# Performance work log

Measured on AMD Instinct MI355X. Metric: run time of the kernel, lower is better.

## Reference

```python
import jax, jax.numpy as jnp
import numpy as np

B, T, D = 2, 1024, 1024
E, H, TOPK = 32, 256, 4
S, HS = 2, H * TOPK  # shared experts, shared hidden dim


def setup_inputs() -> dict:
    key = jax.random.key(0)
    ks = jax.random.split(key, 10)
    sc = 0.02
    return {
        "x": jax.random.normal(ks[0], (B, T, D), dtype=jnp.float32),
        "Wr": jax.random.normal(ks[1], (E, D), dtype=jnp.float32) * sc,
        "router_bias": jnp.zeros((E,), dtype=jnp.float32),
        "Wg": jax.random.normal(ks[2], (E, H, D), dtype=jnp.float32) * sc,
        "Wu": jax.random.normal(ks[3], (E, H, D), dtype=jnp.float32) * sc,
        "Wd": jax.random.normal(ks[4], (E, D, H), dtype=jnp.float32) * sc,
        "Sg": jax.random.normal(ks[5], (S, HS, D), dtype=jnp.float32) * sc,
        "Su": jax.random.normal(ks[6], (S, HS, D), dtype=jnp.float32) * sc,
        "Sd": jax.random.normal(ks[7], (S, D, HS), dtype=jnp.float32) * sc,
    }


def reference(x, Wr, router_bias, Wg, Wu, Wd, Sg, Su, Sd):
    Bx, Tx, Dx = x.shape
    flat = x.reshape(-1, Dx)                      # [N, D]
    N = flat.shape[0]

    # Router: softmax over raw logits, top-k selection on biased logits
    logits = flat @ Wr.T                          # [N, E]
    scores = jax.nn.softmax(logits, axis=-1)
    _, topk_idx = jax.lax.top_k(logits + router_bias, TOPK)   # [N, K]
    topk_scores = jnp.take_along_axis(scores, topk_idx, axis=-1)
    topk_scores = topk_scores / jnp.sum(topk_scores, axis=-1, keepdims=True)

    # Dense per-token per-expert combine weights (0 for unselected experts)
    cw = jnp.zeros((N, E), dtype=flat.dtype).at[
        jnp.arange(N)[:, None], topk_idx
    ].add(topk_scores)                            # [N, E]

    # Routed experts: SwiGLU applied per expert, zero-weighted if unselected
    g = jnp.einsum("nd,ehd->neh", flat, Wg)       # [N, E, H]
    u = jnp.einsum("nd,ehd->neh", flat, Wu)
    h = jax.nn.silu(g) * u
    hw = h * cw[:, :, None]                       # fold combine weight before down-proj
    out = jnp.einsum("neh,edh->nd", hw, Wd)       # [N, D]

    # Shared experts: always active, summed on top
    gs = jnp.einsum("nd,shd->nsh", flat, Sg)      # [N, S, HS]
    us = jnp.einsum("nd,shd->nsh", flat, Su)
    hs = jax.nn.silu(gs) * us
    out = out + jnp.einsum("nsh,sdh->nd", hs, Sd)

    return out.reshape(Bx, Tx, Dx)
```

## Files before the change

### kernel.cpp

```cpp
#include <hip/hip_runtime.h>
#include <hip/hip_bf16.h>


#define N_TOK 2048
#define DDIM 1024
#define NEXP 32
#define HDIM 256
#define TOPK 4
#define NSH 2
#define HSH 1024
#define CNTS 32
#define WM2  96

typedef unsigned short us4 __attribute__((ext_vector_type(4)));
typedef unsigned short us8 __attribute__((ext_vector_type(8)));
typedef short bf16x8 __attribute__((ext_vector_type(8)));
typedef float f32x4 __attribute__((ext_vector_type(4)));

__device__ __forceinline__ unsigned short f2bf(float f) {
  union { float f; unsigned u; } v; v.f = f;
  unsigned r = v.u + 0x7fffu + ((v.u >> 16) & 1u);
  return (unsigned short)(r >> 16);
}
__device__ __forceinline__ float bf2f(unsigned short h) {
  union { unsigned u; float f; } v; v.u = ((unsigned)h) << 16; return v.f;
}
__device__ __forceinline__ uint2 cvt4u(float4 v) {
  union { __hip_bfloat162 b; unsigned u; } a, b2;
  a.b  = __float22bfloat162_rn(make_float2(v.x, v.y));
  b2.b = __float22bfloat162_rn(make_float2(v.z, v.w));
  return make_uint2(a.u, b2.u);
}

__device__ __forceinline__ void pipe_barrier() {
  asm volatile("s_waitcnt lgkmcnt(0)" ::: "memory");
  __builtin_amdgcn_s_barrier();
  __builtin_amdgcn_sched_barrier(0);
}

#define C_X4   524288L
#define C_WG4  2621440L
#define C_WU4  4718592L
#define C_WD4  6815744L
#define C_SG4  7340032L
#define C_SU4  7864320L
#define C_TOT4 8388608L
#define NCVT   16384

__global__ __launch_bounds__(256) void k_prep(const float* __restrict__ x,
                                              const float* __restrict__ Wr,
                                              const float* __restrict__ rb,
                                              const float* __restrict__ Wg,
                                              const float* __restrict__ Wu,
                                              const float* __restrict__ Wd,
                                              const float* __restrict__ Sg,
                                              const float* __restrict__ Su,
                                              const float* __restrict__ Sd,
                                              unsigned short* __restrict__ xb,
                                              unsigned short* __restrict__ Wgb,
                                              unsigned short* __restrict__ Wub,
                                              unsigned short* __restrict__ Wdb,
                                              unsigned short* __restrict__ Sgb,
                                              unsigned short* __restrict__ Sub,
                                              unsigned short* __restrict__ Sdb,
                                              int* __restrict__ cnt,
                                              int* __restrict__ ent,
                                              float* __restrict__ wgt) {
  __shared__ float sX[8 * 1024];
  __shared__ float sLog[8 * 32];
  int tid = threadIdx.x;
  if (blockIdx.x >= 256) {
    long base = (long)(blockIdx.x - 256) * 512;
    const float* s; unsigned short* d; long off;
    if (base < C_WG4) {
      if (base < C_X4)  { s = x;  d = xb;  off = base; }
      else              { s = Wg; d = Wgb; off = base - C_X4; }
    } else if (base < C_WD4) {
      if (base < C_WU4) { s = Wu; d = Wub; off = base - C_WG4; }
      else              { s = Wd; d = Wdb; off = base - C_WU4; }
    } else if (base < C_SU4) {
      if (base < C_SG4) { s = Sg; d = Sgb; off = base - C_WD4; }
      else              { s = Su; d = Sub; off = base - C_SG4; }
    } else              { s = Sd; d = Sdb; off = base - C_SU4; }
    long i0 = off + 2 * tid;
    float4 v0 = reinterpret_cast<const float4*>(s)[i0];
    float4 v1 = reinterpret_cast<const float4*>(s)[i0 + 1];
    uint2 a = cvt4u(v0), b = cvt4u(v1);
    uint4 o = make_uint4(a.x, a.y, b.x, b.y);
    reinterpret_cast<uint4*>(d)[(off >> 1) + tid] = o;
    return;
  }
  int blk = blockIdx.x;
  {
    const float4* xsrc = reinterpret_cast<const float4*>(x + (size_t)blk * 8 * 1024);
    float4* xdst = reinterpret_cast<float4*>(sX);
#pragma unroll
    for (int i = 0; i < 8; i++) xdst[tid + 256 * i] = xsrc[tid + 256 * i];
  }
  __syncthreads();
  int tloc = tid >> 5, e = tid & 31;
  const float4* wr4 = reinterpret_cast<const float4*>(Wr + (size_t)e * DDIM);
  const float* xr = sX + tloc * 1024;
  float acc = 0.f;
#pragma unroll 8
  for (int d4 = 0; d4 < 256; d4++) {
    float4 wv = wr4[d4];
    acc += xr[d4 * 4 + 0] * wv.x + xr[d4 * 4 + 1] * wv.y +
           xr[d4 * 4 + 2] * wv.z + xr[d4 * 4 + 3] * wv.w;
  }
  sLog[tloc * 32 + e] = acc;
  __syncthreads();
  if (tid < 8) {
    int tok = blk * 8 + tid;
    const float* lg = sLog + tid * 32;
    int usedmask = 0;
    int idx[TOPK]; float lv[TOPK];
#pragma unroll
    for (int k = 0; k < TOPK; k++) {
      float best = -3.4e38f; int bi = 0;
      for (int ee = 0; ee < NEXP; ee++) {
        if ((usedmask >> ee) & 1) continue;
        float v = lg[ee] + rb[ee];
        if (v > best) { best = v; bi = ee; }
      }
      usedmask |= 1 << bi; idx[k] = bi; lv[k] = lg[bi];
    }
    float m = fmaxf(fmaxf(lv[0], lv[1]), fmaxf(lv[2], lv[3]));
    float w[TOPK]; float ssum = 0.f;
#pragma unroll
    for (int k = 0; k < TOPK; k++) { w[k] = __expf(lv[k] - m); ssum += w[k]; }
    float inv = 1.f / ssum;
#pragma unroll
    for (int k = 0; k < TOPK; k++) {
      int ee = idx[k];
      int pos = atomicAdd(&cnt[ee * CNTS], 1);
      ent[ee * N_TOK + pos] = tok * TOPK + k;
      wgt[ee * N_TOK + pos] = w[k] * inv;
    }
  }
}

__global__ void k_plan(const int* __restrict__ cnt, int* __restrict__ wk2, int* __restrict__ nwk2) {
  int e = threadIdx.x;
  if (e >= 32) return;
  int ne = cnt[e * CNTS];
  int nt2 = (ne + 127) >> 7;
  int off2 = 0;
  for (int j = 0; j < 32; j++) {
    int v2 = __shfl(nt2, j);
    if (j < e) off2 += v2;
  }
  for (int t = 0; t < nt2; t++) wk2[off2 + t] = e | (t << 8);
  if (e == 31) nwk2[0] = off2 + nt2;
}

__global__ __launch_bounds__(512) void k_gu(const unsigned short* __restrict__ xb,
                                            const unsigned short* __restrict__ Sgb,
                                            const unsigned short* __restrict__ Sub,
                                            const unsigned short* __restrict__ Wgb,
                                            const unsigned short* __restrict__ Wub,
                                            const int* __restrict__ cnt,
                                            const int* __restrict__ ent,
                                            const float* __restrict__ wgt,
                                            unsigned short* __restrict__ hs,
                                            unsigned short* __restrict__ hw,
                                            const int* __restrict__ wk2,
                                            const int* __restrict__ nwk2) {
  __shared__ unsigned short sPool[2 * 128 * 40 + 2 * 256 * 40];
  __shared__ int sTok[128];
  __shared__ float sW[128];
  int tid = threadIdx.x, lane = tid & 63, wid = tid >> 6;
  int wm = wid >> 2, wn = wid & 3;
  int b = blockIdx.x;

  if (b < 256) {
    int xg = b & 15, mt = b >> 4;
    int s = xg >> 3, ht = xg & 7;
    unsigned short* sA = sPool;
    unsigned short* sB = sPool + 2 * 128 * 40;

    int ar = tid >> 2, akc = tid & 3;
    const unsigned short* aSrc = xb + (size_t)(mt * 128 + ar) * DDIM + akc * 8;
    int aOff = ar * 40 + akc * 8;
    const unsigned short* bSrc[2];
    int bOff[2];
#pragma unroll
    for (int p = 0; p < 2; p++) {
      int c = tid + p * 512;
      int row = c >> 2, kc = c & 3;
      int sel = (row >> 4) & 1;
      int h = ht * 128 + ((row >> 5) << 4) + (row & 15);
      bSrc[p] = (sel ? Sub : Sgb) + (size_t)(s * HSH + h) * DDIM + kc * 8;
      bOff[p] = row * 40 + kc * 8;
    }

    us8 aReg = *reinterpret_cast<const us8*>(aSrc);
    us8 bReg[2];
#pragma unroll
    for (int p = 0; p < 2; p++) bReg[p] = *reinterpret_cast<const us8*>(bSrc[p]);

    f32x4 acc[4][4];
#pragma unroll
    for (int mf = 0; mf < 4; mf++)
#pragma unroll
      for (int nf = 0; nf < 4; nf++) acc[mf][nf] = {0.f, 0.f, 0.f, 0.f};

    int cur = 0;
    for (int step = 0; step < 32; ++step) {
      *reinterpret_cast<us8*>(&sA[cur * 5120 + aOff]) = aReg;
#pragma unroll
      for (int p = 0; p < 2; p++) *reinterpret_cast<us8*>(&sB[cur * 10240 + bOff[p]]) = bReg[p];
      if (step < 31) {
        int k0 = (step + 1) * 32;
        aReg = *reinterpret_cast<const us8*>(aSrc + k0);
#pragma unroll
        for (int p = 0; p < 2; p++) bReg[p] = *reinterpret_cast<const us8*>(bSrc[p] + k0);
      }
      pipe_barrier();
      int ka = (lane >> 4) * 8;
      bf16x8 a[4];
#pragma unroll
      for (int mf = 0; mf < 4; mf++)
        a[mf] = *reinterpret_cast<const bf16x8*>(&sA[cur * 5120 + (wm * 64 + mf * 16 + (lane & 15)) * 40 + ka]);
#pragma unroll
      for (int nf = 0; nf < 4; nf++) {
        bf16x8 bb = *reinterpret_cast<const bf16x8*>(&sB[cur * 10240 + (wn * 64 + nf * 16 + (lane & 15)) * 40 + ka]);
#pragma unroll
        for (int mf = 0; mf < 4; mf++)
          acc[mf][nf] = __builtin_amdgcn_mfma_f32_16x16x32_bf16(a[mf], bb, acc[mf][nf], 0, 0, 0);
      }
      cur ^= 1;
    }
#pragma unroll
    for (int mf = 0; mf < 4; mf++) {
#pragma unroll
      for (int t = 0; t < 2; t++) {
#pragma unroll
        for (int r = 0; r < 4; r++) {
          int tok = mt * 128 + wm * 64 + mf * 16 + ((lane >> 4) << 2) + r;
          float g = acc[mf][2 * t][r], u = acc[mf][2 * t + 1][r];
          float hval = (g / (1.f + __expf(-g))) * u;
          int h = ht * 128 + (wn * 2 + t) * 16 + (lane & 15);
          hs[(size_t)(tok * NSH + s) * HSH + h] = f2bf(hval);
        }
      }
    }
    return;
  }

  int idx = b - 256;
  int widx = idx >> 2, ht = idx & 3;
  if (widx >= nwk2[0]) return;
  int item = wk2[widx];
  int e = item & 255, mt = item >> 8;
  int ne = cnt[e * CNTS];
  unsigned short* sA = sPool;
  unsigned short* sB = sPool + 2 * 128 * 40;
  if (tid < 128) {
    int pos = mt * 128 + tid;
    int p2 = min(pos, ne - 1);
    sTok[tid] = ent[e * N_TOK + p2];
    sW[tid] = (pos < ne) ? wgt[e * N_TOK + p2] : 0.f;
  }
  __syncthreads();

  int ar = tid >> 2, akc = tid & 3;
  const unsigned short* aSrc = xb + (size_t)(sTok[ar] >> 2) * DDIM + akc * 8;
  int aOff = ar * 40 + akc * 8;
  int br = tid >> 2, bkc = tid & 3;
  int sel = (br >> 4) & 1;
  int h = ht * 64 + ((br >> 5) << 4) + (br & 15);
  const unsigned short* bSrc = (sel ? Wub : Wgb) + (size_t)(e * HDIM + h) * DDIM + bkc * 8;
  int bOff = br * 40 + bkc * 8;

  us8 aReg = *reinterpret_cast<const us8*>(aSrc);
  us8 bReg = *reinterpret_cast<const us8*>(bSrc);

  f32x4 acc[4][2];
#pragma unroll
  for (int mf = 0; mf < 4; mf++)
#pragma unroll
    for (int nf = 0; nf < 2; nf++) acc[mf][nf] = {0.f, 0.f, 0.f, 0.f};

  int cur = 0;
  for (int step = 0; step < 32; ++step) {
    *reinterpret_cast<us8*>(&sA[cur * 5120 + aOff]) = aReg;
    *reinterpret_cast<us8*>(&sB[cur * 5120 + bOff]) = bReg;
    if (step < 31) {
      int k0 = (step + 1) * 32;
      aReg = *reinterpret_cast<const us8*>(aSrc + k0);
      bReg = *reinterpret_cast<const us8*>(bSrc + k0);
    }
    pipe_barrier();
    int ka = (lane >> 4) * 8;
    bf16x8 a[4];
#pragma unroll
    for (int mf = 0; mf < 4; mf++)
      a[mf] = *reinterpret_cast<const bf16x8*>(&sA[cur * 5120 + (wm * 64 + mf * 16 + (lane & 15)) * 40 + ka]);
#pragma unroll
    for (int nf = 0; nf < 2; nf++) {
      bf16x8 bb = *reinterpret_cast<const bf16x8*>(&sB[cur * 5120 + (wn * 32 + nf * 16 + (lane & 15)) * 40 + ka]);
#pragma unroll
      for (int mf = 0; mf < 4; mf++)
        acc[mf][nf] = __builtin_amdgcn_mfma_f32_16x16x32_bf16(a[mf], bb, acc[mf][nf], 0, 0, 0);
    }
    cur ^= 1;
  }
#pragma unroll
  for (int mf = 0; mf < 4; mf++) {
#pragma unroll
    for (int r = 0; r < 4; r++) {
      int tl = wm * 64 + mf * 16 + ((lane >> 4) << 2) + r;
      int pos = mt * 128 + tl;
      if (pos < ne) {
        float g = acc[mf][0][r], u = acc[mf][1][r];
        float hval = (g / (1.f + __expf(-g))) * u * sW[tl];
        int ts = sTok[tl];
        int hcol = ht * 64 + wn * 16 + (lane & 15);
        hw[(size_t)ts * HDIM + hcol] = f2bf(hval);
      }
    }
  }
}

__global__ __launch_bounds__(512) void k_down(const unsigned short* __restrict__ hs,
                                              const unsigned short* __restrict__ Sdb,
                                              const unsigned short* __restrict__ hw,
                                              const unsigned short* __restrict__ Wdb,
                                              const int* __restrict__ cnt,
                                              const int* __restrict__ ent,
                                              unsigned short* __restrict__ Psh,
                                              unsigned short* __restrict__ Pslot,
                                              const int* __restrict__ wk2,
                                              const int* __restrict__ nwk2) {
  __shared__ unsigned short sPool[4 * 128 * 40];
  __shared__ int sTok[128];
  int tid = threadIdx.x, lane = tid & 63, wid = tid >> 6;
  int wm = wid >> 2, wn = wid & 3;
  int b = blockIdx.x;
  unsigned short* sA = sPool;
  unsigned short* sB = sPool + 2 * 128 * 40;

  if (b < 256) {
    int xg = b & 15, mt = b >> 4;
    int dh = xg >> 1, s = xg & 1;

    int ar = tid >> 2, akc = tid & 3;
    const unsigned short* aSrc = hs + (size_t)((mt * 128 + ar) * NSH + s) * HSH + akc * 8;
    int aOff = ar * 40 + akc * 8;
    int br = tid >> 2, bkc = tid & 3;
    const unsigned short* bSrc = Sdb + (size_t)(s * DDIM + dh * 128 + br) * HSH + bkc * 8;
    int bOff = br * 40 + bkc * 8;

    us8 aReg = *reinterpret_cast<const us8*>(aSrc);
    us8 bReg = *reinterpret_cast<const us8*>(bSrc);

    f32x4 acc[4][2];
#pragma unroll
    for (int mf = 0; mf < 4; mf++)
#pragma unroll
      for (int nf = 0; nf < 2; nf++) acc[mf][nf] = {0.f, 0.f, 0.f, 0.f};

    int cur = 0;
    for (int step = 0; step < 32; ++step) {
      *reinterpret_cast<us8*>(&sA[cur * 5120 + aOff]) = aReg;
      *reinterpret_cast<us8*>(&sB[cur * 5120 + bOff]) = bReg;
      if (step < 31) {
        int k0 = (step + 1) * 32;
        aReg = *reinterpret_cast<const us8*>(aSrc + k0);
        bReg = *reinterpret_cast<const us8*>(bSrc + k0);
      }
      pipe_barrier();
      int ka = (lane >> 4) * 8;
      bf16x8 a[4];
#pragma unroll
      for (int mf = 0; mf < 4; mf++)
        a[mf] = *reinterpret_cast<const bf16x8*>(&sA[cur * 5120 + (wm * 64 + mf * 16 + (lane & 15)) * 40 + ka]);
#pragma unroll
      for (int nf = 0; nf < 2; nf++) {
        bf16x8 bb = *reinterpret_cast<const bf16x8*>(&sB[cur * 5120 + (wn * 32 + nf * 16 + (lane & 15)) * 40 + ka]);
#pragma unroll
        for (int mf = 0; mf < 4; mf++)
          acc[mf][nf] = __builtin_amdgcn_mfma_f32_16x16x32_bf16(a[mf], bb, acc[mf][nf], 0, 0, 0);
      }
      cur ^= 1;
    }
#pragma unroll
    for (int mf = 0; mf < 4; mf++) {
#pragma unroll
      for (int nf = 0; nf < 2; nf++) {
#pragma unroll
        for (int r = 0; r < 4; r++) {
          int tok = mt * 128 + wm * 64 + mf * 16 + ((lane >> 4) << 2) + r;
          int d = dh * 128 + wn * 32 + nf * 16 + (lane & 15);
          Psh[(size_t)s * N_TOK * DDIM + (size_t)tok * DDIM + d] = f2bf(acc[mf][nf][r]);
        }
      }
    }
    return;
  }

  int idx = b - 256;
  int widx = idx >> 3, dh = idx & 7;
  if (widx >= nwk2[0]) return;
  int item = wk2[widx];
  int e = item & 255, mt = item >> 8;
  int ne = cnt[e * CNTS];
  if (tid < 128) {
    int pos = mt * 128 + tid;
    int p2 = min(pos, ne - 1);
    sTok[tid] = ent[e * N_TOK + p2];
  }
  __syncthreads();

  int ar = tid >> 2, akc = tid & 3;
  const unsigned short* aSrc = hw + (size_t)sTok[ar] * HDIM + akc * 8;
  int aOff = ar * 40 + akc * 8;
  int br = tid >> 2, bkc = tid & 3;
  int d0 = dh * 128 + br;
  const unsigned short* bSrc = Wdb + (size_t)(e * DDIM + d0) * HDIM + bkc * 8;
  int bOff = br * 40 + bkc * 8;

  us8 aReg = *reinterpret_cast<const us8*>(aSrc);
  us8 bReg = *reinterpret_cast<const us8*>(bSrc);

  f32x4 acc[4][2];
#pragma unroll
  for (int mf = 0; mf < 4; mf++)
#pragma unroll
    for (int nf = 0; nf < 2; nf++) acc[mf][nf] = {0.f, 0.f, 0.f, 0.f};

  int cur = 0;
  for (int step = 0; step < 8; ++step) {
    *reinterpret_cast<us8*>(&sA[cur * 5120 + aOff]) = aReg;
    *reinterpret_cast<us8*>(&sB[cur * 5120 + bOff]) = bReg;
    if (step < 7) {
      int k0 = (step + 1) * 32;
      aReg = *reinterpret_cast<const us8*>(aSrc + k0);
      bReg = *reinterpret_cast<const us8*>(bSrc + k0);
    }
    pipe_barrier();
    int ka = (lane >> 4) * 8;
    bf16x8 a[4];
#pragma unroll
    for (int mf = 0; mf < 4; mf++)
      a[mf] = *reinterpret_cast<const bf16x8*>(&sA[cur * 5120 + (wm * 64 + mf * 16 + (lane & 15)) * 40 + ka]);
#pragma unroll
    for (int nf = 0; nf < 2; nf++) {
      bf16x8 bb = *reinterpret_cast<const bf16x8*>(&sB[cur * 5120 + (wn * 32 + nf * 16 + (lane & 15)) * 40 + ka]);
#pragma unroll
      for (int mf = 0; mf < 4; mf++)
        acc[mf][nf] = __builtin_amdgcn_mfma_f32_16x16x32_bf16(a[mf], bb, acc[mf][nf], 0, 0, 0);
    }
    cur ^= 1;
  }
#pragma unroll
  for (int mf = 0; mf < 4; mf++) {
#pragma unroll
    for (int nf = 0; nf < 2; nf++) {
#pragma unroll
      for (int r = 0; r < 4; r++) {
        int tl = wm * 64 + mf * 16 + ((lane >> 4) << 2) + r;
        int pos = mt * 128 + tl;
        if (pos < ne) {
          int ts = sTok[tl];
          int d = dh * 128 + wn * 32 + nf * 16 + (lane & 15);
          Pslot[(size_t)ts * DDIM + d] = f2bf(acc[mf][nf][r]);
        }
      }
    }
  }
}

__global__ __launch_bounds__(256) void k_combine(const unsigned short* __restrict__ Pslot,
                                                 const unsigned short* __restrict__ Psh,
                                                 float* __restrict__ out) {
  int i = blockIdx.x * 256 + threadIdx.x;
  int base = i * 8;
  int tok = base >> 10, d = base & 1023;
  const us8 p0 = *reinterpret_cast<const us8*>(Pslot + ((size_t)tok * 4 + 0) * DDIM + d);
  const us8 p1 = *reinterpret_cast<const us8*>(Pslot + ((size_t)tok * 4 + 1) * DDIM + d);
  const us8 p2 = *reinterpret_cast<const us8*>(Pslot + ((size_t)tok * 4 + 2) * DDIM + d);
  const us8 p3 = *reinterpret_cast<const us8*>(Pslot + ((size_t)tok * 4 + 3) * DDIM + d);
  const us8 q0 = *reinterpret_cast<const us8*>(Psh + (size_t)base);
  const us8 q1 = *reinterpret_cast<const us8*>(Psh + (size_t)N_TOK * DDIM + base);
  float o[8];
#pragma unroll
  for (int j = 0; j < 8; j++)
    o[j] = bf2f(p0[j]) + bf2f(p1[j]) + bf2f(p2[j]) + bf2f(p3[j]) + bf2f(q0[j]) + bf2f(q1[j]);
  float4 v0 = {o[0], o[1], o[2], o[3]};
  float4 v1 = {o[4], o[5], o[6], o[7]};
  reinterpret_cast<float4*>(out + base)[0] = v0;
  reinterpret_cast<float4*>(out + base)[1] = v1;
}

extern "C" void kernel_launch(void* const* d_in, const int* in_sizes, int n_in,
                              void* d_out, int out_size, void* d_ws, size_t ws_size,
                              hipStream_t stream) {
  const float* x  = (const float*)d_in[0];
  const float* Wr = (const float*)d_in[1];
  const float* rb = (const float*)d_in[2];
  const float* Wg = (const float*)d_in[3];
  const float* Wu = (const float*)d_in[4];
  const float* Wd = (const float*)d_in[5];
  const float* Sg = (const float*)d_in[6];
  const float* Su = (const float*)d_in[7];
  const float* Sd = (const float*)d_in[8];
  float* out = (float*)d_out;
  char* w = (char*)d_ws;

  unsigned short* xb    = (unsigned short*)(w + (size_t)0);
  unsigned short* Wgb   = (unsigned short*)(w + ((size_t)4  << 20));
  unsigned short* Wub   = (unsigned short*)(w + ((size_t)20 << 20));
  unsigned short* Wdb   = (unsigned short*)(w + ((size_t)36 << 20));
  unsigned short* Sgb   = (unsigned short*)(w + ((size_t)52 << 20));
  unsigned short* Sub   = (unsigned short*)(w + ((size_t)56 << 20));
  unsigned short* Sdb   = (unsigned short*)(w + ((size_t)60 << 20));
  unsigned short* hw    = (unsigned short*)(w + ((size_t)64 << 20));
  unsigned short* hs    = (unsigned short*)(w + ((size_t)68 << 20));
  unsigned short* Pslot = (unsigned short*)(w + ((size_t)76 << 20));
  unsigned short* Psh   = (unsigned short*)(w + ((size_t)92 << 20));
  int*   cnt = (int*)(w + ((size_t)100 << 20));
  int*   ent = (int*)(w + ((size_t)100 << 20) + 8192);
  float* wgt = (float*)(w + ((size_t)100 << 20) + 8192 + (size_t)NEXP * N_TOK * 4);
  int*   wk2  = (int*)(w + ((size_t)102 << 20));
  int*   nwk2 = (int*)(w + ((size_t)102 << 20) + 4096);

  hipMemsetAsync(cnt, 0, NEXP * CNTS * sizeof(int), stream);

  k_prep<<<256 + NCVT, 256, 0, stream>>>(x, Wr, rb, Wg, Wu, Wd, Sg, Su, Sd,
                                         xb, Wgb, Wub, Wdb, Sgb, Sub, Sdb,
                                         cnt, ent, wgt);
  k_plan<<<1, 64, 0, stream>>>(cnt, wk2, nwk2);

  k_gu<<<256 + WM2 * 4, 512, 0, stream>>>(xb, Sgb, Sub, Wgb, Wub, cnt, ent, wgt,
                                          hs, hw, wk2, nwk2);
  k_down<<<256 + WM2 * 8, 512, 0, stream>>>(hs, Sdb, hw, Wdb, cnt, ent,
                                            Psh, Pslot, wk2, nwk2);

  k_combine<<<N_TOK * DDIM / (256 * 8), 256, 0, stream>>>(Pslot, Psh, out);
}
```

Baseline: 136.9 us.

## Move down-projection weight conversion from prep kernel into gate/up kernel

The fp32-to-bf16 conversion of Wd and Sd moves out of k_prep and into extra trailing blocks of k_gu. Those blocks can run alongside the gate/up GEMM tiles. This shortens the critical prep stage that routing and gate/up wait on, since the down weights are only needed by k_down. The extra blocks compete with the GEMM for bandwidth and compute units. GU_GEMM is fixed at 640, so the GEMM block count must still match 256 + WM2*4.

New measurement: 141.4 us. +3.3%, slower.

```diff
diff --git a/kernel.cpp b/kernel.cpp
--- a/kernel.cpp
+++ b/kernel.cpp
@@ -41,28 +41,22 @@
 #define C_X4   524288L
 #define C_WG4  2621440L
 #define C_WU4  4718592L
-#define C_WD4  6815744L
-#define C_SG4  7340032L
-#define C_SU4  7864320L
-#define C_TOT4 8388608L
-#define NCVT   16384
+#define C_SG4  5242880L
+#define C_SU4  5767168L
+#define NCVT   11264
 
 __global__ __launch_bounds__(256) void k_prep(const float* __restrict__ x,
                                               const float* __restrict__ Wr,
                                               const float* __restrict__ rb,
                                               const float* __restrict__ Wg,
                                               const float* __restrict__ Wu,
-                                              const float* __restrict__ Wd,
                                               const float* __restrict__ Sg,
                                               const float* __restrict__ Su,
-                                              const float* __restrict__ Sd,
                                               unsigned short* __restrict__ xb,
                                               unsigned short* __restrict__ Wgb,
                                               unsigned short* __restrict__ Wub,
-                                              unsigned short* __restrict__ Wdb,
                                               unsigned short* __restrict__ Sgb,
                                               unsigned short* __restrict__ Sub,
-                                              unsigned short* __restrict__ Sdb,
                                               int* __restrict__ cnt,
                                               int* __restrict__ ent,
                                               float* __restrict__ wgt) {
@@ -75,13 +69,10 @@
     if (base < C_WG4) {
       if (base < C_X4)  { s = x;  d = xb;  off = base; }
       else              { s = Wg; d = Wgb; off = base - C_X4; }
-    } else if (base < C_WD4) {
+    } else if (base < C_SG4) {
       if (base < C_WU4) { s = Wu; d = Wub; off = base - C_WG4; }
-      else              { s = Wd; d = Wdb; off = base - C_WU4; }
-    } else if (base < C_SU4) {
-      if (base < C_SG4) { s = Sg; d = Sgb; off = base - C_WD4; }
-      else              { s = Su; d = Sub; off = base - C_SG4; }
-    } else              { s = Sd; d = Sdb; off = base - C_SU4; }
+      else              { s = Sg; d = Sgb; off = base - C_WU4; }
+    } else              { s = Su; d = Sub; off = base - C_SG4; }
     long i0 = off + 2 * tid;
     float4 v0 = reinterpret_cast<const float4*>(s)[i0];
     float4 v1 = reinterpret_cast<const float4*>(s)[i0 + 1];
@@ -154,11 +145,20 @@
   if (e == 31) nwk2[0] = off2 + nt2;
 }
 
+#define GU_GEMM 640
+#define D_WD4   2097152L
+#define D_TOT4  2621440L
+#define NCVT2   2560
+
 __global__ __launch_bounds__(512) void k_gu(const unsigned short* __restrict__ xb,
                                             const unsigned short* __restrict__ Sgb,
                                             const unsigned short* __restrict__ Sub,
                                             const unsigned short* __restrict__ Wgb,
                                             const unsigned short* __restrict__ Wub,
+                                            const float* __restrict__ Wd,
+                                            const float* __restrict__ Sd,
+                                            unsigned short* __restrict__ Wdb,
+                                            unsigned short* __restrict__ Sdb,
                                             const int* __restrict__ cnt,
                                             const int* __restrict__ ent,
                                             const float* __restrict__ wgt,
@@ -172,6 +172,20 @@
   int tid = threadIdx.x, lane = tid & 63, wid = tid >> 6;
   int wm = wid >> 2, wn = wid & 3;
   int b = blockIdx.x;
+
+  if (b >= GU_GEMM) {
+    long base = (long)(b - GU_GEMM) * 1024;
+    const float* s; unsigned short* d; long off;
+    if (base < D_WD4) { s = Wd; d = Wdb; off = base; }
+    else              { s = Sd; d = Sdb; off = base - D_WD4; }
+    long i0 = off + 2 * tid;
+    float4 v0 = reinterpret_cast<const float4*>(s)[i0];
+    float4 v1 = reinterpret_cast<const float4*>(s)[i0 + 1];
+    uint2 a = cvt4u(v0), bb = cvt4u(v1);
+    uint4 o = make_uint4(a.x, a.y, bb.x, bb.y);
+    reinterpret_cast<uint4*>(d)[(off >> 1) + tid] = o;
+    return;
+  }
 
   if (b < 256) {
     int xg = b & 15, mt = b >> 4;
@@ -528,13 +542,13 @@
 
   hipMemsetAsync(cnt, 0, NEXP * CNTS * sizeof(int), stream);
 
-  k_prep<<<256 + NCVT, 256, 0, stream>>>(x, Wr, rb, Wg, Wu, Wd, Sg, Su, Sd,
-                                         xb, Wgb, Wub, Wdb, Sgb, Sub, Sdb,
+  k_prep<<<256 + NCVT, 256, 0, stream>>>(x, Wr, rb, Wg, Wu, Sg, Su,
+                                         xb, Wgb, Wub, Sgb, Sub,
                                          cnt, ent, wgt);
   k_plan<<<1, 64, 0, stream>>>(cnt, wk2, nwk2);
 
-  k_gu<<<256 + WM2 * 4, 512, 0, stream>>>(xb, Sgb, Sub, Wgb, Wub, cnt, ent, wgt,
-                                          hs, hw, wk2, nwk2);
+  k_gu<<<GU_GEMM + NCVT2, 512, 0, stream>>>(xb, Sgb, Sub, Wgb, Wub, Wd, Sd, Wdb, Sdb,
+                                            cnt, ent, wgt, hs, hw, wk2, nwk2);
   k_down<<<256 + WM2 * 8, 512, 0, stream>>>(hs, Sdb, hw, Wdb, cnt, ent,
                                             Psh, Pslot, wk2, nwk2);
 
```
